# Optimization experiments

Hardware: AMD Instinct MI355X
Metric: run time of the kernel (lower is better)

Reference implementation:

```python
import jax, jax.numpy as jnp
import numpy as np


def _rotate_half(x):
    a, b = jnp.split(x, 2, axis=-1)
    return jnp.concatenate([-b, a], axis=-1)


def _rope_tables(L, d, dtype):
    inv = 1.0 / (10000.0 ** (jnp.arange(0, d, 2, dtype=jnp.float32) / d))
    ang = jnp.arange(L, dtype=jnp.float32)[:, None] * inv[None, :]  # (L, d/2)
    cos = jnp.repeat(jnp.cos(ang), 2, axis=-1)[None, :, None, :].astype(dtype)  # (1,L,1,d)
    sin = jnp.repeat(jnp.sin(ang), 2, axis=-1)[None, :, None, :].astype(dtype)
    return cos, sin


def setup_inputs() -> dict:
    key = jax.random.key(0)
    ks = jax.random.split(key, 7)
    B, L, D, h = 1, 1024, 768, 12
    d = D // h
    s = 0.02
    return {
        "X": jax.random.normal(ks[0], (B, L, D), jnp.float32),
        "Wq": jax.random.normal(ks[1], (D, D), jnp.float32) * s,
        "Wk": jax.random.normal(ks[2], (D, D), jnp.float32) * s,
        "Wv": jax.random.normal(ks[3], (D, D), jnp.float32) * s,
        "Wu": jax.random.normal(ks[4], (D, D), jnp.float32) * s,
        "Wg": jax.random.normal(ks[5], (3 * h, D), jnp.float32) * s,
        "Wo": jax.random.normal(ks[6], (D, D), jnp.float32) * s,
        "prior_mu": jnp.zeros((1, 1, h, d), jnp.float32),
        "prior_log_tau": jnp.zeros((1, 1, h, 1), jnp.float32),
    }


def _forward(X, Wq, Wk, Wv, Wu, Wg, Wo, prior_mu, prior_log_tau):
    B, L, D = X.shape
    h = prior_mu.shape[2]
    d = D // h
    eps = 1e-12
    # projections (torch Linear: x @ W.T, no bias)
    q = (X @ Wq.T).reshape(B, L, h, d)
    k = (X @ Wk.T).reshape(B, L, h, d)
    v = (X @ Wv.T).reshape(B, L, h, d)
    u = (X @ Wu.T).reshape(B, L, h, d)
    gate = (X @ Wg.T).reshape(B, L, h, 3)
    t = jnp.arange(1, L + 1, dtype=X.dtype).reshape(1, L, 1, 1)
    # calculate_logit (logit_type='deviation', causal)
    log_tau = jnp.exp(jnp.clip(prior_log_tau, -50.0, 30.0))
    u_sum = jnp.cumsum(u, axis=1)
    bar_u = (log_tau * prior_mu + u_sum) / (log_tau + t)
    s_i = -jnp.sum(u * bar_u, axis=-1, keepdims=True) / np.float32(np.sqrt(d))  # (B,L,h,1)
    # RoPE + L2 normalize q, k
    cos, sin = _rope_tables(L, d, X.dtype)
    q = q * cos + _rotate_half(q) * sin
    k = k * cos + _rotate_half(k) * sin
    q = q / jnp.maximum(jnp.linalg.norm(q, axis=-1, keepdims=True), eps)
    k = k / jnp.maximum(jnp.linalg.norm(k, axis=-1, keepdims=True), eps)
    # associative causal branch of compute_o
    s_max = jax.lax.stop_gradient(jnp.max(s_i, axis=1, keepdims=True))
    exp_s = jnp.exp(s_i - s_max)              # (B,L,h,1)
    E_t = jnp.cumsum(exp_s, axis=1)
    P_t = jnp.cumsum(s_i, axis=1)
    kv = jnp.einsum('blhd,blhe->blhde', k, v)  # (B,L,h,d,d)
    F_t = jnp.cumsum(exp_s[..., None] * kv, axis=1)
    G_t = jnp.cumsum(s_i[..., None] * kv, axis=1)
    H_t = jnp.cumsum(kv, axis=1)
    sig1 = jax.nn.sigmoid(gate[..., 0:1])      # (B,L,h,1)
    sigh = jax.nn.sigmoid(gate[..., 1:2])
    alpha = sigh / (E_t + eps)
    beta = (sig1 - sigh) / t
    gamma = -((beta * P_t + sigh) / t)
    M = alpha[..., None] * F_t + beta[..., None] * G_t + gamma[..., None] * H_t
    out = jnp.einsum('blhd,blhde->blhe', q, M)  # (B,L,h,d)
    # LayerNorm over head dim, eps=1e-5, no affine
    mu = jnp.mean(out, axis=-1, keepdims=True)
    var = jnp.mean(jnp.square(out - mu), axis=-1, keepdims=True)
    out = (out - mu) / jnp.sqrt(var + 1e-5)
    # output projection (dropout=0.0 -> identity)
    return out.reshape(B, L, D) @ Wo.T


def reference(X, Wq, Wk, Wv, Wu, Wg, Wo, prior_mu, prior_log_tau):
    return _forward(X, Wq, Wk, Wv, Wu, Wg, Wo, prior_mu, prior_log_tau)
```

## Files before the change

kernel.cpp:

```cpp
#include <hip/hip_runtime.h>
#include <hip/hip_bf16.h>
#include <math.h>

typedef __attribute__((ext_vector_type(8))) short bf16x8;
typedef __attribute__((ext_vector_type(4))) float f32x4;

#define SEQ 1024
#define DIM 768
#define NH 12
#define HD 64


__device__ __forceinline__ float wave_reduce_sum(float v) {
    for (int off = 1; off < 64; off <<= 1) v += __shfl_xor(v, off);
    return v;
}
__device__ __forceinline__ short f2bs(float x) {
    __hip_bfloat16 h = __float2bfloat16(x);
    return *reinterpret_cast<short*>(&h);
}
__device__ __forceinline__ float bs2f(short x) {
    __hip_bfloat16 h = *reinterpret_cast<__hip_bfloat16*>(&x);
    return (float)h;
}
__device__ __forceinline__ bf16x8 cvt8r(const float4& a, const float4& b) {
    bf16x8 r;
    r[0]=f2bs(a.x); r[1]=f2bs(a.y); r[2]=f2bs(a.z); r[3]=f2bs(a.w);
    r[4]=f2bs(b.x); r[5]=f2bs(b.y); r[6]=f2bs(b.z); r[7]=f2bs(b.w);
    return r;
}
__device__ __forceinline__ void async_copy16(const void* gptr, void* ldsbase, int lane) {
#if __has_builtin(__builtin_amdgcn_global_load_lds)
    __builtin_amdgcn_global_load_lds(
        (const __attribute__((address_space(1))) unsigned int*)gptr,
        (__attribute__((address_space(3))) unsigned int*)ldsbase, 16, 0, 0);
#else
    *(bf16x8*)((short*)ldsbase + lane*8) = *(const bf16x8*)gptr;
#endif
}

__global__ __launch_bounds__(256) void k_prep(const float* __restrict__ X,
    const float* __restrict__ Wq, const float* __restrict__ Wk,
    const float* __restrict__ Wv, const float* __restrict__ Wu,
    const float* __restrict__ Wg, const float* __restrict__ Wo,
    short* __restrict__ Xb, short* __restrict__ Wqb, short* __restrict__ Wkb,
    short* __restrict__ Wvb, short* __restrict__ Wub, short* __restrict__ Wgb,
    short* __restrict__ Wob)
{
    int seg = blockIdx.y;
    const float* src; short* dst; int n8;
    switch (seg) {
        case 0: src = X;  dst = Xb;  n8 = 98304; break;
        case 1: src = Wq; dst = Wqb; n8 = 73728; break;
        case 2: src = Wk; dst = Wkb; n8 = 73728; break;
        case 3: src = Wv; dst = Wvb; n8 = 73728; break;
        case 4: src = Wu; dst = Wub; n8 = 73728; break;
        case 5: src = Wg; dst = Wgb; n8 = 3456;  break;
        default: src = Wo; dst = Wob; n8 = 73728; break;
    }
    int i = blockIdx.x*256 + threadIdx.x;
    if (i >= n8) return;
    const float* s = src + (size_t)i*8;
    *(bf16x8*)(dst + (size_t)i*8) = cvt8r(*(const float4*)s, *(const float4*)(s + 4));
}

__global__ __launch_bounds__(256, 3) void k_proj5(const short* __restrict__ Xb,
    const short* __restrict__ Wqb, const short* __restrict__ Wkb,
    const short* __restrict__ Wvb, const short* __restrict__ Wub,
    const short* __restrict__ Wgb,
    __hip_bfloat16* __restrict__ Qb, __hip_bfloat16* __restrict__ Kb,
    __hip_bfloat16* __restrict__ Vt, __hip_bfloat16* __restrict__ Ub,
    float* __restrict__ G)
{
    int t = blockIdx.x;
    int mat, rt, ct;
    if (t < 288)      { int m3 = t/96; mat = (m3==2)?3:m3; int r = t%96; rt = r/6; ct = r%6; }
    else if (t < 384) { mat = 2; int r = t-288; rt = r/8; ct = r%8; }
    else              { mat = 4; rt = t-384; ct = 0; }

    __shared__ short lds[24576];

    int tid = threadIdx.x;
    int wv = tid>>6, lane = tid&63, g = lane>>4, n = lane&15;
    int wn = wv;

    const short* Asrc; const short* Bsrc; int arow0, brow0, Brows;
    if (mat == 2) { Asrc = Wvb; Bsrc = Xb; arow0 = rt*64; brow0 = ct*128; Brows = SEQ; }
    else {
        Asrc = Xb; arow0 = rt*64; brow0 = ct*128;
        Bsrc = (mat==0)?Wqb:(mat==1)?Wkb:(mat==3)?Wub:Wgb;
        Brows = (mat==4) ? 36 : DIM;
    }

    auto dma_step = [&](int buf, int k0) {
        short* Ab = lds + buf*4096;
        short* Bb = lds + 8192 + buf*8192;
        for (int p = 0; p < 2; ++p) {
            int sbase = p*256 + wv*64;
            int s = sbase + lane;
            int r = s >> 3, c = s & 7, cl = c ^ (r & 7);
            async_copy16(Asrc + (size_t)(arow0 + r)*DIM + k0 + cl*8, Ab + sbase*8, lane);
        }
        for (int p = 0; p < 4; ++p) {
            int sbase = p*256 + wv*64;
            int s = sbase + lane;
            int r = s >> 3, c = s & 7, cl = c ^ (r & 7);
            int gr = brow0 + r; if (gr >= Brows) gr = Brows - 1;
            async_copy16(Bsrc + (size_t)gr*DIM + k0 + cl*8, Bb + sbase*8, lane);
        }
    };

    f32x4 acc[4][2];
    for (int i=0;i<4;++i) for (int j=0;j<2;++j) acc[i][j] = (f32x4){0,0,0,0};

    dma_step(0, 0);
    for (int it = 0; it < 12; ++it) {
        __syncthreads();
        if (it < 11) dma_step(1 - (it & 1), (it + 1)*64);
        int buf = it & 1;
        const short* Ab = lds + buf*4096;
        const short* Bb = lds + 8192 + buf*8192;
        for (int ks = 0; ks < 2; ++ks) {
            int q = ks*4 + g;
            bf16x8 af[4], bfr[2];
            for (int i=0;i<4;++i)
                af[i] = *(const bf16x8*)(&Ab[((i*16+n)*8 + (q ^ (n&7)))*8]);
            for (int j=0;j<2;++j)
                bfr[j] = *(const bf16x8*)(&Bb[((wn*32+j*16+n)*8 + (q ^ (n&7)))*8]);
            for (int i=0;i<4;++i)
                for (int j=0;j<2;++j)
                    acc[i][j] = __builtin_amdgcn_mfma_f32_16x16x32_bf16(af[i], bfr[j], acc[i][j], 0,0,0);
        }
    }
    __syncthreads();

    if (mat == 4) {
        for (int i=0;i<4;++i) for (int j=0;j<2;++j) for (int r=0;r<4;++r) {
            int row = rt*64 + i*16 + g*4 + r;
            int col = wn*32 + j*16 + n;
            if (col < 36) G[(size_t)row*36 + col] = acc[i][j][r];
        }
        return;
    }

    short* C = lds;
    for (int i=0;i<4;++i) for (int j=0;j<2;++j) for (int r=0;r<4;++r)
        C[(i*16 + g*4 + r)*128 + wn*32 + j*16 + n] = f2bs(acc[i][j][r]);
    __syncthreads();

    if (mat == 2) {
        for (int k = 0; k < 16; ++k) {
            int row = k*4 + wv;
            unsigned int v = ((const unsigned int*)C)[row*64 + lane];
            ((unsigned int*)(Vt + (size_t)(rt*64 + row)*SEQ + ct*128))[lane] = v;
        }
    } else if (mat == 3) {
        for (int k = 0; k < 32; ++k) {
            int u = k*4 + wv;
            int row = u >> 1, hsel = u & 1;
            Ub[((size_t)(2*ct + hsel)*SEQ + rt*64 + row)*HD + lane] =
                *(__hip_bfloat16*)&C[row*128 + hsel*64 + lane];
        }
    } else {
        __hip_bfloat16* dst = (mat==0) ? Qb : Kb;
        int i2 = lane >> 1;
        float inv = expf((float)i2 * (-9.210340371976184f / 32.f));
        for (int k = 0; k < 32; ++k) {
            int u = k*4 + wv;
            int row = u >> 1, hsel = u & 1;
            int l = rt*64 + row;
            float x = bs2f(C[row*128 + hsel*64 + lane]);
            float ang = (float)l * inv;
            float c = cosf(ang), s = sinf(ang);
            float p = __shfl(x, lane ^ 32);
            float rot = (lane < 32) ? -p : p;
            float y = x*c + rot*s;
            float nrm = wave_reduce_sum(y*y);
            y = y / fmaxf(sqrtf(nrm), 1e-12f);
            dst[((size_t)(2*ct + hsel)*SEQ + l)*HD + lane] = __float2bfloat16(y);
        }
    }
}

__global__ __launch_bounds__(1024) void k_scan(const __hip_bfloat16* __restrict__ Ub,
    const float* __restrict__ G, const float* __restrict__ pmu,
    const float* __restrict__ plt,
    float* __restrict__ si_, float* __restrict__ es_, float* __restrict__ al_,
    float* __restrict__ be_, float* __restrict__ ga_)
{
    int h = blockIdx.x;
    int tid = threadIdx.x, wv = tid >> 6, lane = tid & 63;
    __shared__ float sbuf[SEQ], ebuf[SEQ], g1b[SEQ], ghb[SEQ];
    __shared__ float stot[16][64];
    __shared__ float wmax[16];
    __shared__ float smax_s;

    float ltv = fminf(fmaxf(plt[h], -50.f), 30.f);
    float ltau = expf(ltv);
    float mu = pmu[h*HD + lane];

    const __hip_bfloat16* up = Ub + ((size_t)h*SEQ + wv*64)*HD + lane;
    float Ul = 0.f;
    for (int i = 0; i < 64; ++i) Ul += (float)up[(size_t)i*HD];
    stot[wv][lane] = Ul;
    __syncthreads();
    float pre = ltau * mu;
    for (int w2 = 0; w2 < wv; ++w2) pre += stot[w2][lane];
    float V = pre;
    for (int i = 0; i < 64; ++i) {
        float uv = (float)up[(size_t)i*HD];
        V += uv;
        int l = wv*64 + i;
        float bar = V / (ltau + (float)(l + 1));
        float p = wave_reduce_sum(uv * bar);
        if (lane == 0) sbuf[l] = -p * 0.125f;
    }
    __syncthreads();
    float v = sbuf[tid];
    float vm = v;
    for (int off = 1; off < 64; off <<= 1) vm = fmaxf(vm, __shfl_xor(vm, off));
    if (lane == 0) wmax[wv] = vm;
    __syncthreads();
    if (wv == 0) {
        float mm = (lane < 16) ? wmax[lane] : -1e30f;
        for (int off = 1; off < 16; off <<= 1) mm = fmaxf(mm, __shfl_xor(mm, off));
        if (lane == 0) smax_s = mm;
    }
    __syncthreads();
    float ev = expf(fminf(v - smax_s, 0.f));
    ebuf[tid] = ev;
    g1b[tid] = 1.f / (1.f + expf(-G[(size_t)tid*36 + h*3 + 0]));
    ghb[tid] = 1.f / (1.f + expf(-G[(size_t)tid*36 + h*3 + 1]));
    si_[h*SEQ + tid] = v;
    es_[h*SEQ + tid] = ev;
    __syncthreads();
    if (wv == 0) {
        int base = lane * 16;
        float se = 0.f, ss = 0.f;
        for (int i = 0; i < 16; ++i) { se += ebuf[base + i]; ss += sbuf[base + i]; }
        float pe = se, ps = ss;
        for (int off = 1; off < 64; off <<= 1) {
            float t1 = __shfl_up(pe, off), t2 = __shfl_up(ps, off);
            if (lane >= off) { pe += t1; ps += t2; }
        }
        float E = pe - se, P = ps - ss;
        for (int i = 0; i < 16; ++i) {
            int l = base + i;
            E += ebuf[l]; P += sbuf[l];
            float t = (float)(l + 1);
            float s1 = g1b[l], sh = ghb[l];
            float a = sh / (E + 1e-12f);
            float b = (s1 - sh) / t;
            float gm = -((b * P + sh) / t);
            al_[h*SEQ + l] = a;
            be_[h*SEQ + l] = b;
            ga_[h*SEQ + l] = gm;
        }
    }
}

__global__ __launch_bounds__(256) void k_attn(const __hip_bfloat16* __restrict__ Qb,
    const __hip_bfloat16* __restrict__ Kb, const __hip_bfloat16* __restrict__ Vt,
    const float* __restrict__ si_, const float* __restrict__ es_,
    const float* __restrict__ al_, const float* __restrict__ be_,
    const float* __restrict__ ga_, __hip_bfloat16* __restrict__ opre)
{
    int t = blockIdx.x, h = blockIdx.y;
    int wv = threadIdx.x >> 6, lane = threadIdx.x & 63;
    int g = lane >> 4, n = lane & 15;
    __shared__ short P[4][16*64];
    __shared__ float Op[4][16][64];
    short* Pw = P[wv];
    int m0 = t*16;
    const short* qrow = (const short*)Qb + ((size_t)h*SEQ + m0 + n)*HD + g*8;
    bf16x8 qa0 = *(const bf16x8*)qrow;
    bf16x8 qa1 = *(const bf16x8*)(qrow + 32);
    const float* al = al_ + h*SEQ;
    const float* be = be_ + h*SEQ;
    const float* ga = ga_ + h*SEQ;
    const float* es = es_ + h*SEQ;
    const float* si = si_ + h*SEQ;
    float A_[4], B_[4], G_[4];
    for (int r = 0; r < 4; ++r) {
        int m = m0 + g*4 + r;
        A_[r] = al[m]; B_[r] = be[m]; G_[r] = ga[m];
    }
    f32x4 acco[4];
    for (int et = 0; et < 4; ++et) acco[et] = (f32x4){0.f,0.f,0.f,0.f};

    int jtmax = t >> 2;
    for (int jt = wv; jt <= jtmax; jt += 4) {
        int j0 = jt*64;
        for (int ct = 0; ct < 4; ++ct) {
            const short* krow = (const short*)Kb + ((size_t)h*SEQ + j0 + ct*16 + n)*HD + g*8;
            bf16x8 kb0 = *(const bf16x8*)krow;
            bf16x8 kb1 = *(const bf16x8*)(krow + 32);
            f32x4 sacc = {0.f,0.f,0.f,0.f};
            sacc = __builtin_amdgcn_mfma_f32_16x16x32_bf16(qa0, kb0, sacc, 0, 0, 0);
            sacc = __builtin_amdgcn_mfma_f32_16x16x32_bf16(qa1, kb1, sacc, 0, 0, 0);
            int j = j0 + ct*16 + n;
            float ej = es[j], sj = si[j];
            int chunk = ct*2 + (n>>3), e = n&7;
            for (int r = 0; r < 4; ++r) {
                int m = m0 + g*4 + r;
                float w = (j <= m) ? (A_[r]*ej + B_[r]*sj + G_[r]) : 0.f;
                int ml = g*4 + r;
                Pw[ml*64 + (chunk ^ (ml&7))*8 + e] = f2bs(w * sacc[r]);
            }
        }
        const short* vb = (const short*)Vt + (size_t)h*HD*SEQ;
        for (int et = 0; et < 4; ++et) {
            for (int sub = 0; sub < 2; ++sub) {
                int q = sub*4 + g;
                bf16x8 pa = *(const bf16x8*)(&Pw[n*64 + (q ^ (n&7))*8]);
                bf16x8 vfr = *(const bf16x8*)(vb + (size_t)(et*16 + n)*SEQ + j0 + sub*32 + g*8);
                acco[et] = __builtin_amdgcn_mfma_f32_16x16x32_bf16(pa, vfr, acco[et], 0, 0, 0);
            }
        }
    }
    for (int et = 0; et < 4; ++et)
        for (int r = 0; r < 4; ++r)
            Op[wv][g*4 + r][et*16 + n] = acco[et][r];
    __syncthreads();
    for (int rr = 0; rr < 4; ++rr) {
        int row = wv*4 + rr;
        float v = Op[0][row][lane] + Op[1][row][lane] + Op[2][row][lane] + Op[3][row][lane];
        float sm = wave_reduce_sum(v);
        float sq = wave_reduce_sum(v*v);
        float mu = sm * (1.f/64.f);
        float var = fmaxf(sq * (1.f/64.f) - mu*mu, 0.f);
        float invs = rsqrtf(var + 1e-5f);
        opre[(size_t)(m0 + row)*DIM + h*HD + lane] = __float2bfloat16((v - mu) * invs);
    }
}

__global__ __launch_bounds__(256, 4) void k_oproj(const short* __restrict__ A,
    const short* __restrict__ Wob, float* __restrict__ out)
{
    int rt = blockIdx.x, ct = blockIdx.y;
    __shared__ short lds[16384];

    int tid = threadIdx.x;
    int wv = tid>>6, lane = tid&63, g = lane>>4, n = lane&15;
    int wm = wv>>1, wn = wv&1;

    auto dma_step = [&](int buf, int k0) {
        short* Ab = lds + buf*4096;
        short* Bb = lds + 8192 + buf*4096;
        for (int p = 0; p < 2; ++p) {
            int sbase = p*256 + wv*64;
            int s = sbase + lane;
            int r = s >> 3, c = s & 7, cl = c ^ (r & 7);
            async_copy16(A + (size_t)(rt*64 + r)*DIM + k0 + cl*8, Ab + sbase*8, lane);
            async_copy16(Wob + (size_t)(ct*64 + r)*DIM + k0 + cl*8, Bb + sbase*8, lane);
        }
    };

    f32x4 acc[2][2];
    for (int i=0;i<2;++i) for (int j=0;j<2;++j) acc[i][j] = (f32x4){0,0,0,0};

    dma_step(0, 0);
    for (int it = 0; it < 12; ++it) {
        __syncthreads();
        if (it < 11) dma_step(1 - (it & 1), (it + 1)*64);
        int buf = it & 1;
        const short* Ab = lds + buf*4096;
        const short* Bb = lds + 8192 + buf*4096;
        for (int ks = 0; ks < 2; ++ks) {
            int q = ks*4 + g;
            bf16x8 af[2], bfr[2];
            for (int i=0;i<2;++i)
                af[i] = *(const bf16x8*)(&Ab[((wm*32+i*16+n)*8 + (q ^ (n&7)))*8]);
            for (int j=0;j<2;++j)
                bfr[j] = *(const bf16x8*)(&Bb[((wn*32+j*16+n)*8 + (q ^ (n&7)))*8]);
            for (int i=0;i<2;++i)
                for (int j=0;j<2;++j)
                    acc[i][j] = __builtin_amdgcn_mfma_f32_16x16x32_bf16(af[i], bfr[j], acc[i][j], 0,0,0);
        }
    }
    for (int i=0;i<2;++i) for (int j=0;j<2;++j) for (int r=0;r<4;++r) {
        int row = rt*64 + wm*32 + i*16 + g*4 + r;
        int col = ct*64 + wn*32 + j*16 + n;
        out[(size_t)row*DIM + col] = acc[i][j][r];
    }
}

extern "C" void kernel_launch(void* const* d_in, const int* in_sizes, int n_in,
                              void* d_out, int out_size, void* d_ws, size_t ws_size,
                              hipStream_t stream) {
    const float* X   = (const float*)d_in[0];
    const float* Wq  = (const float*)d_in[1];
    const float* Wk  = (const float*)d_in[2];
    const float* Wv  = (const float*)d_in[3];
    const float* Wu  = (const float*)d_in[4];
    const float* Wg  = (const float*)d_in[5];
    const float* Wo  = (const float*)d_in[6];
    const float* pmu = (const float*)d_in[7];
    const float* plt = (const float*)d_in[8];

    char* w = (char*)d_ws;
    __hip_bfloat16* Qb   = (__hip_bfloat16*)(w + 0);
    __hip_bfloat16* Kb   = (__hip_bfloat16*)(w + 1572864);
    __hip_bfloat16* Vt   = (__hip_bfloat16*)(w + 3145728);
    __hip_bfloat16* opre = (__hip_bfloat16*)(w + 4718592);
    float*          G    = (float*)(w + 6291456);
    float*          si_  = (float*)(w + 6438912);
    float*          es_  = si_ + NH*SEQ;
    float*          al_  = es_ + NH*SEQ;
    float*          be_  = al_ + NH*SEQ;
    float*          ga_  = be_ + NH*SEQ;
    short*          Xb   = (short*)(w + 6684672);
    short*          Wqb  = (short*)(w + 8257536);
    short*          Wkb  = (short*)(w + 9437184);
    short*          Wvb  = (short*)(w + 10616832);
    short*          Wub  = (short*)(w + 11796480);
    short*          Wgb  = (short*)(w + 12976128);
    short*          Wob  = (short*)(w + 13031424);
    __hip_bfloat16* Ub   = (__hip_bfloat16*)d_out;
    float*          out  = (float*)d_out;

    hipLaunchKernelGGL(k_prep, dim3(384, 7), dim3(256), 0, stream,
                       X, Wq, Wk, Wv, Wu, Wg, Wo, Xb, Wqb, Wkb, Wvb, Wub, Wgb, Wob);
    hipLaunchKernelGGL(k_proj5, dim3(400), dim3(256), 0, stream,
                       Xb, Wqb, Wkb, Wvb, Wub, Wgb, Qb, Kb, Vt, Ub, G);
    hipLaunchKernelGGL(k_scan, dim3(NH), dim3(1024), 0, stream,
                       Ub, G, pmu, plt, si_, es_, al_, be_, ga_);
    hipLaunchKernelGGL(k_attn, dim3(64, NH), dim3(256), 0, stream,
                       Qb, Kb, Vt, si_, es_, al_, be_, ga_, opre);
    hipLaunchKernelGGL(k_oproj, dim3(16, 12), dim3(256), 0, stream,
                       (const short*)opre, Wob, out);
}
```

Before: 170.8 us.

## Recast s_i scan as causal MFMA Gram product and precompute RoPE table

Replaces the 12-block sequential cumulative-sum scan for s_i with a parallel kernel. It computes s_i as a causal sum of dot products u_l·u_j via MFMA tiles, and each of the 16x12 blocks covers 64 rows. The remaining scan (max, exp, prefix sums, gate coefficients) moves into a small one-wave-per-head kernel. RoPE cos/sin values are also precomputed once into a table in the prep kernel instead of calling cosf/sinf per element in the projection epilogue. This trades O(L·d) serial work for O(L²·d) parallel MFMA work, adds a kernel launch, and changes how rounding accumulates.

```diff
diff --git a/kernel.cpp b/kernel.cpp
--- a/kernel.cpp
+++ b/kernel.cpp
@@ -45,9 +45,21 @@
     const float* __restrict__ Wg, const float* __restrict__ Wo,
     short* __restrict__ Xb, short* __restrict__ Wqb, short* __restrict__ Wkb,
     short* __restrict__ Wvb, short* __restrict__ Wub, short* __restrict__ Wgb,
-    short* __restrict__ Wob)
+    short* __restrict__ Wob, float2* __restrict__ rope)
 {
     int seg = blockIdx.y;
+    if (seg == 7) {
+        int i = blockIdx.x*256 + threadIdx.x;
+        if (i >= 32768) return;
+        int l = i >> 5, i2 = i & 31;
+        float inv = expf((float)i2 * (-9.210340371976184f / 32.f));
+        float ang = (float)l * inv;
+        float2 cs;
+        cs.x = cosf(ang);
+        cs.y = sinf(ang);
+        rope[i] = cs;
+        return;
+    }
     const float* src; short* dst; int n8;
     switch (seg) {
         case 0: src = X;  dst = Xb;  n8 = 98304; break;
@@ -70,7 +82,7 @@
     const short* __restrict__ Wgb,
     __hip_bfloat16* __restrict__ Qb, __hip_bfloat16* __restrict__ Kb,
     __hip_bfloat16* __restrict__ Vt, __hip_bfloat16* __restrict__ Ub,
-    float* __restrict__ G)
+    float* __restrict__ G, const float2* __restrict__ rope)
 {
     int t = blockIdx.x;
     int mat, rt, ct;
@@ -164,17 +176,15 @@
     } else {
         __hip_bfloat16* dst = (mat==0) ? Qb : Kb;
         int i2 = lane >> 1;
-        float inv = expf((float)i2 * (-9.210340371976184f / 32.f));
         for (int k = 0; k < 32; ++k) {
             int u = k*4 + wv;
             int row = u >> 1, hsel = u & 1;
             int l = rt*64 + row;
             float x = bs2f(C[row*128 + hsel*64 + lane]);
-            float ang = (float)l * inv;
-            float c = cosf(ang), s = sinf(ang);
+            float2 cs = rope[l*32 + i2];
             float p = __shfl(x, lane ^ 32);
             float rot = (lane < 32) ? -p : p;
-            float y = x*c + rot*s;
+            float y = x*cs.x + rot*cs.y;
             float nrm = wave_reduce_sum(y*y);
             y = y / fmaxf(sqrtf(nrm), 1e-12f);
             dst[((size_t)(2*ct + hsel)*SEQ + l)*HD + lane] = __float2bfloat16(y);
@@ -182,80 +192,99 @@
     }
 }
 
-__global__ __launch_bounds__(1024) void k_scan(const __hip_bfloat16* __restrict__ Ub,
-    const float* __restrict__ G, const float* __restrict__ pmu,
-    const float* __restrict__ plt,
-    float* __restrict__ si_, float* __restrict__ es_, float* __restrict__ al_,
-    float* __restrict__ be_, float* __restrict__ ga_)
-{
-    int h = blockIdx.x;
-    int tid = threadIdx.x, wv = tid >> 6, lane = tid & 63;
-    __shared__ float sbuf[SEQ], ebuf[SEQ], g1b[SEQ], ghb[SEQ];
-    __shared__ float stot[16][64];
-    __shared__ float wmax[16];
-    __shared__ float smax_s;
+__global__ __launch_bounds__(256) void k_si(const __hip_bfloat16* __restrict__ Ub,
+    const float* __restrict__ pmu, const float* __restrict__ plt,
+    float* __restrict__ si_)
+{
+    int T = blockIdx.x, h = blockIdx.y;
+    int wv = threadIdx.x >> 6, lane = threadIdx.x & 63;
+    int g = lane >> 4, n = lane & 15;
+    int lbase = T*64 + wv*16;
+    const short* ub = (const short*)Ub + (size_t)h*SEQ*HD;
+
+    bf16x8 a0 = *(const bf16x8*)(ub + (size_t)(lbase + n)*HD + g*8);
+    bf16x8 a1 = *(const bf16x8*)(ub + (size_t)(lbase + n)*HD + 32 + g*8);
 
     float ltv = fminf(fmaxf(plt[h], -50.f), 30.f);
     float ltau = expf(ltv);
-    float mu = pmu[h*HD + lane];
-
-    const __hip_bfloat16* up = Ub + ((size_t)h*SEQ + wv*64)*HD + lane;
-    float Ul = 0.f;
-    for (int i = 0; i < 64; ++i) Ul += (float)up[(size_t)i*HD];
-    stot[wv][lane] = Ul;
-    __syncthreads();
-    float pre = ltau * mu;
-    for (int w2 = 0; w2 < wv; ++w2) pre += stot[w2][lane];
-    float V = pre;
-    for (int i = 0; i < 64; ++i) {
-        float uv = (float)up[(size_t)i*HD];
-        V += uv;
-        int l = wv*64 + i;
-        float bar = V / (ltau + (float)(l + 1));
-        float p = wave_reduce_sum(uv * bar);
-        if (lane == 0) sbuf[l] = -p * 0.125f;
-    }
-    __syncthreads();
-    float v = sbuf[tid];
-    float vm = v;
+
+    float p[4];
+    for (int r = 0; r < 4; ++r) {
+        int l = lbase + g*4 + r;
+        float acc = 0.f;
+        for (int c = n; c < 64; c += 16)
+            acc += bs2f(ub[(size_t)l*HD + c]) * pmu[h*HD + c];
+        p[r] = ltau * acc;
+    }
+
+    int diag = 4*T + wv;
+    for (int jt = 0; jt < diag; ++jt) {
+        const short* br = ub + (size_t)(jt*16 + n)*HD + g*8;
+        bf16x8 b0 = *(const bf16x8*)br;
+        bf16x8 b1 = *(const bf16x8*)(br + 32);
+        f32x4 sacc = {0.f,0.f,0.f,0.f};
+        sacc = __builtin_amdgcn_mfma_f32_16x16x32_bf16(a0, b0, sacc, 0,0,0);
+        sacc = __builtin_amdgcn_mfma_f32_16x16x32_bf16(a1, b1, sacc, 0,0,0);
+        for (int r = 0; r < 4; ++r) p[r] += sacc[r];
+    }
+    {
+        const short* br = ub + (size_t)(diag*16 + n)*HD + g*8;
+        bf16x8 b0 = *(const bf16x8*)br;
+        bf16x8 b1 = *(const bf16x8*)(br + 32);
+        f32x4 sacc = {0.f,0.f,0.f,0.f};
+        sacc = __builtin_amdgcn_mfma_f32_16x16x32_bf16(a0, b0, sacc, 0,0,0);
+        sacc = __builtin_amdgcn_mfma_f32_16x16x32_bf16(a1, b1, sacc, 0,0,0);
+        for (int r = 0; r < 4; ++r) if (n <= g*4 + r) p[r] += sacc[r];
+    }
+    for (int off = 1; off < 16; off <<= 1)
+        for (int r = 0; r < 4; ++r) p[r] += __shfl_xor(p[r], off);
+
+    if (n == 0) {
+        for (int r = 0; r < 4; ++r) {
+            int l = lbase + g*4 + r;
+            si_[h*SEQ + l] = -p[r] * 0.125f / (ltau + (float)(l + 1));
+        }
+    }
+}
+
+__global__ __launch_bounds__(64) void k_scan2(const float* __restrict__ G,
+    const float* __restrict__ si_, float* __restrict__ es_,
+    float* __restrict__ al_, float* __restrict__ be_, float* __restrict__ ga_)
+{
+    int h = blockIdx.x, lane = threadIdx.x;
+    const float* si = si_ + h*SEQ;
+    int base = lane * 16;
+    float sv[16], ev[16];
+    float vm = -1e30f;
+#pragma unroll
+    for (int i = 0; i < 16; ++i) { sv[i] = si[base + i]; vm = fmaxf(vm, sv[i]); }
     for (int off = 1; off < 64; off <<= 1) vm = fmaxf(vm, __shfl_xor(vm, off));
-    if (lane == 0) wmax[wv] = vm;
-    __syncthreads();
-    if (wv == 0) {
-        float mm = (lane < 16) ? wmax[lane] : -1e30f;
-        for (int off = 1; off < 16; off <<= 1) mm = fmaxf(mm, __shfl_xor(mm, off));
-        if (lane == 0) smax_s = mm;
-    }
-    __syncthreads();
-    float ev = expf(fminf(v - smax_s, 0.f));
-    ebuf[tid] = ev;
-    g1b[tid] = 1.f / (1.f + expf(-G[(size_t)tid*36 + h*3 + 0]));
-    ghb[tid] = 1.f / (1.f + expf(-G[(size_t)tid*36 + h*3 + 1]));
-    si_[h*SEQ + tid] = v;
-    es_[h*SEQ + tid] = ev;
-    __syncthreads();
-    if (wv == 0) {
-        int base = lane * 16;
-        float se = 0.f, ss = 0.f;
-        for (int i = 0; i < 16; ++i) { se += ebuf[base + i]; ss += sbuf[base + i]; }
-        float pe = se, ps = ss;
-        for (int off = 1; off < 64; off <<= 1) {
-            float t1 = __shfl_up(pe, off), t2 = __shfl_up(ps, off);
-            if (lane >= off) { pe += t1; ps += t2; }
-        }
-        float E = pe - se, P = ps - ss;
-        for (int i = 0; i < 16; ++i) {
-            int l = base + i;
-            E += ebuf[l]; P += sbuf[l];
-            float t = (float)(l + 1);
-            float s1 = g1b[l], sh = ghb[l];
-            float a = sh / (E + 1e-12f);
-            float b = (s1 - sh) / t;
-            float gm = -((b * P + sh) / t);
-            al_[h*SEQ + l] = a;
-            be_[h*SEQ + l] = b;
-            ga_[h*SEQ + l] = gm;
-        }
+    float se = 0.f, ss = 0.f;
+#pragma unroll
+    for (int i = 0; i < 16; ++i) {
+        ev[i] = expf(fminf(sv[i] - vm, 0.f));
+        se += ev[i]; ss += sv[i];
+    }
+    float pe = se, ps = ss;
+    for (int off = 1; off < 64; off <<= 1) {
+        float t1 = __shfl_up(pe, off), t2 = __shfl_up(ps, off);
+        if (lane >= off) { pe += t1; ps += t2; }
+    }
+    float E = pe - se, P = ps - ss;
+#pragma unroll
+    for (int i = 0; i < 16; ++i) {
+        int l = base + i;
+        E += ev[i]; P += sv[i];
+        float t = (float)(l + 1);
+        float s1 = 1.f / (1.f + expf(-G[(size_t)l*36 + h*3 + 0]));
+        float sh = 1.f / (1.f + expf(-G[(size_t)l*36 + h*3 + 1]));
+        float a = sh / (E + 1e-12f);
+        float b = (s1 - sh) / t;
+        float gm = -((b * P + sh) / t);
+        es_[h*SEQ + l] = ev[i];
+        al_[h*SEQ + l] = a;
+        be_[h*SEQ + l] = b;
+        ga_[h*SEQ + l] = gm;
     }
 }
 
@@ -416,15 +445,18 @@
     short*          Wub  = (short*)(w + 11796480);
     short*          Wgb  = (short*)(w + 12976128);
     short*          Wob  = (short*)(w + 13031424);
+    float2*         rope = (float2*)(w + 14680064);
     __hip_bfloat16* Ub   = (__hip_bfloat16*)d_out;
     float*          out  = (float*)d_out;
 
-    hipLaunchKernelGGL(k_prep, dim3(384, 7), dim3(256), 0, stream,
-                       X, Wq, Wk, Wv, Wu, Wg, Wo, Xb, Wqb, Wkb, Wvb, Wub, Wgb, Wob);
+    hipLaunchKernelGGL(k_prep, dim3(384, 8), dim3(256), 0, stream,
+                       X, Wq, Wk, Wv, Wu, Wg, Wo, Xb, Wqb, Wkb, Wvb, Wub, Wgb, Wob, rope);
     hipLaunchKernelGGL(k_proj5, dim3(400), dim3(256), 0, stream,
-                       Xb, Wqb, Wkb, Wvb, Wub, Wgb, Qb, Kb, Vt, Ub, G);
-    hipLaunchKernelGGL(k_scan, dim3(NH), dim3(1024), 0, stream,
-                       Ub, G, pmu, plt, si_, es_, al_, be_, ga_);
+                       Xb, Wqb, Wkb, Wvb, Wub, Wgb, Qb, Kb, Vt, Ub, G, rope);
+    hipLaunchKernelGGL(k_si, dim3(16, NH), dim3(256), 0, stream,
+                       Ub, pmu, plt, si_);
+    hipLaunchKernelGGL(k_scan2, dim3(NH), dim3(64), 0, stream,
+                       G, si_, es_, al_, be_, ga_);
     hipLaunchKernelGGL(k_attn, dim3(64, NH), dim3(256), 0, stream,
                        Qb, Kb, Vt, si_, es_, al_, be_, ga_, opre);
     hipLaunchKernelGGL(k_oproj, dim3(16, 12), dim3(256), 0, stream,
```

Measured after the change: 161.6 us. 5.4% less time.
